# Kernel tuning notes

Hardware: AMD Instinct MI355X
Metric: run time of the kernel (lower is better)

The kernel has to match this reference:

```python
import jax, jax.numpy as jnp
import numpy as np

NUM_CLASSES = 80
TOPK = 13          # TaskAlignedAssigner topk
TAL_ALPHA = 1.0    # alignment = score^alpha * iou^beta
TAL_BETA = 6.0
VFL_ALPHA = 0.75   # varifocal loss
VFL_GAMMA = 2.0
CLS_W, IOU_W = 1.0, 2.5
EPS = 1e-9


def batch_iou(box1, box2, eps=1e-9):
    """box1 [B,M1,4], box2 [B,M2,4] (xyxy) -> iou [B,M1,M2]."""
    b1 = box1[:, :, None, :]
    b2 = box2[:, None, :, :]
    x1y1 = jnp.maximum(b1[..., :2], b2[..., :2])
    x2y2 = jnp.minimum(b1[..., 2:], b2[..., 2:])
    overlap = jnp.clip(x2y2 - x1y1, 0).prod(-1)
    area1 = jnp.clip(b1[..., 2:] - b1[..., :2], 0).prod(-1)
    area2 = jnp.clip(b2[..., 2:] - b2[..., :2], 0).prod(-1)
    return overlap / (area1 + area2 - overlap + eps)


def check_points_inside(points, bboxes, eps=EPS):
    """points [L,2], bboxes [B,n,4] -> [B,n,L] float (1 = anchor center inside gt)."""
    x = points[None, None, :, 0]
    y = points[None, None, :, 1]
    xmin, ymin, xmax, ymax = (bboxes[..., i:i + 1] for i in range(4))
    inside = jnp.minimum(jnp.minimum(x - xmin, y - ymin),
                         jnp.minimum(xmax - x, ymax - y)) > eps
    return inside.astype(bboxes.dtype)


def giou_loss(pb, gb, eps=1e-10):
    """Elementwise 1 - GIoU for xyxy boxes [..., 4]."""
    px1, py1, px2, py2 = (pb[..., i] for i in range(4))
    gx1, gy1, gx2, gy2 = (gb[..., i] for i in range(4))
    x1 = jnp.maximum(px1, gx1); y1 = jnp.maximum(py1, gy1)
    x2 = jnp.minimum(px2, gx2); y2 = jnp.minimum(py2, gy2)
    overlap = jnp.clip(x2 - x1, 0) * jnp.clip(y2 - y1, 0)
    area_p = jnp.clip(px2 - px1, 0) * jnp.clip(py2 - py1, 0)
    area_g = jnp.clip(gx2 - gx1, 0) * jnp.clip(gy2 - gy1, 0)
    union = area_p + area_g - overlap + eps
    iou = overlap / union
    cx1 = jnp.minimum(px1, gx1); cy1 = jnp.minimum(py1, gy1)
    cx2 = jnp.maximum(px2, gx2); cy2 = jnp.maximum(py2, gy2)
    c = jnp.clip(cx2 - cx1, 0) * jnp.clip(cy2 - cy1, 0) + eps
    return 1.0 - (iou - (c - union) / c)


def task_aligned_assign(pred_scores, pred_bboxes, anchor_points,
                        gt_labels, gt_bboxes, pad_gt_mask):
    """TaskAlignedAssigner.forward (no-grad in torch). Returns assigned
    labels [B,L], bboxes [B,L,4], scores [B,L,C], pos mask [B,L] float."""
    B, L, C = pred_scores.shape
    n = gt_bboxes.shape[1]
    ious = batch_iou(gt_bboxes, pred_bboxes)                       # [B,n,L]
    gl = gt_labels[..., 0]                                         # [B,n]
    # gather predicted class prob for each gt's class -> [B,n,L]
    scores_gt = jnp.take_along_axis(jnp.swapaxes(pred_scores, 1, 2),
                                    gl[:, :, None], axis=1)
    align = (scores_gt ** TAL_ALPHA) * (ious ** TAL_BETA)          # [B,n,L]
    is_in_gts = check_points_inside(anchor_points, gt_bboxes)      # [B,n,L]
    metrics = align * is_in_gts
    _, topk_idxs = jax.lax.top_k(metrics, TOPK)                    # [B,n,K]
    b_idx = jnp.arange(B)[:, None, None]
    n_idx = jnp.arange(n)[None, :, None]
    is_in_topk = jnp.zeros_like(metrics).at[b_idx, n_idx, topk_idxs].set(1.0)
    is_in_topk = is_in_topk * pad_gt_mask
    mask_pos = is_in_topk * is_in_gts * pad_gt_mask                # [B,n,L]
    mps = mask_pos.sum(1)                                          # [B,L]
    # anchors matched to >1 gt: keep only the max-iou gt
    is_max_iou = jnp.swapaxes(
        jax.nn.one_hot(ious.argmax(1), n, dtype=ious.dtype), 1, 2) # [B,n,L]
    mask_pos = jnp.where((mps > 1)[:, None, :], is_max_iou, mask_pos)
    mps = mask_pos.sum(1)                                          # [B,L]
    agi = mask_pos.argmax(1)                                       # [B,L]
    bi = jnp.arange(B)[:, None]
    assigned_labels = jnp.where(mps > 0, gl[bi, agi], NUM_CLASSES)
    assigned_bboxes = gt_bboxes[bi, agi]                           # [B,L,4]
    assigned_scores = jax.nn.one_hot(assigned_labels, C + 1,
                                     dtype=pred_scores.dtype)[..., :C]
    # rescale by alignment metric
    align = align * mask_pos
    max_metrics = align.max(-1, keepdims=True)                     # [B,n,1]
    max_ious = (ious * mask_pos).max(-1, keepdims=True)            # [B,n,1]
    align = align / (max_metrics + EPS) * max_ious
    assigned_scores = assigned_scores * align.max(1)[..., None]
    pos = (mps > 0).astype(pred_scores.dtype)
    return assigned_labels, assigned_bboxes, assigned_scores, pos


def setup_inputs() -> dict:
    key = jax.random.key(0)
    ks = jax.random.split(key, 6)
    B, N, C = 32, 100, NUM_CLASSES
    # anchor centers for strides 8/16/32 on a 640x640 image -> L = 8400
    pts = []
    for s in (8, 16, 32):
        g = 640 // s
        xs = (np.arange(g, dtype=np.float32) + 0.5) * s
        xv, yv = np.meshgrid(xs, xs)
        pts.append(np.stack([xv.ravel(), yv.ravel()], -1))
    anchor_points = jnp.asarray(np.concatenate(pts, 0))            # [8400,2]
    L = anchor_points.shape[0]

    def rand_boxes(k, lead):
        k1, k2 = jax.random.split(k)
        cxy = jax.random.uniform(k1, lead + (2,)) * 640.0
        wh = jax.random.uniform(k2, lead + (2,)) * 120.0 + 8.0
        return jnp.clip(jnp.concatenate([cxy - wh / 2, cxy + wh / 2], -1), 0.0, 640.0)

    pred_scores = jax.random.uniform(ks[0], (B, L, C), minval=1e-4, maxval=1.0 - 1e-4)
    pred_bboxes = rand_boxes(ks[1], (B, L))
    gt_bboxes = rand_boxes(ks[2], (B, N))
    gt_labels = jax.random.randint(ks[3], (B, N, 1), 0, C)
    num_gt = jax.random.randint(ks[4], (B, 1, 1), 20, N + 1)
    pad_gt_mask = (jnp.arange(N)[None, :, None] < num_gt).astype(jnp.float32)
    return {"pred_scores": pred_scores, "pred_bboxes": pred_bboxes,
            "anchor_points": anchor_points, "gt_labels": gt_labels,
            "gt_bboxes": gt_bboxes, "pad_gt_mask": pad_gt_mask}


def reference(pred_scores, pred_bboxes, anchor_points, gt_labels, gt_bboxes, pad_gt_mask):
    # --- assignment (torch runs it under no_grad) ---
    al, ab, asc, pos = jax.tree_util.tree_map(
        jax.lax.stop_gradient,
        task_aligned_assign(jax.lax.stop_gradient(pred_scores),
                            jax.lax.stop_gradient(pred_bboxes),
                            anchor_points, gt_labels, gt_bboxes, pad_gt_mask))
    asc_sum = jnp.maximum(asc.sum(), 1.0)
    # --- varifocal classification loss ---
    one_hot_label = jax.nn.one_hot(al, NUM_CLASSES + 1, dtype=pred_scores.dtype)[..., :NUM_CLASSES]
    w = VFL_ALPHA * (pred_scores ** VFL_GAMMA) * (1.0 - one_hot_label) + asc * one_hot_label
    p = jnp.clip(pred_scores, EPS, 1.0 - EPS)
    bce = -(asc * jnp.log(p) + (1.0 - asc) * jnp.log1p(-p))
    loss_cls = (bce * w).sum() / asc_sum
    # --- GIoU bbox loss on positive anchors, score-weighted ---
    bbox_weight = asc.sum(-1) * pos                                # [B,L]
    loss_iou = (giou_loss(pred_bboxes, ab) * bbox_weight).sum() / asc_sum
    return CLS_W * loss_cls + IOU_W * loss_iou
```

## Files before the change

### kernel.cpp

```cpp
#include <hip/hip_runtime.h>

#define NB 32
#define NGT 100
#define NL 8400
#define NC 80
#define KTOP 13
#define MAXC 640
#define NROWS (NB * NL)
#define TK_BLOCKS (NB * NGT / 4)
#define F_BLOCKS 2048
#define CR_BLOCKS (NROWS / 256)
#define SC_BLOCKS_X 33
#define TOTAL4 ((unsigned)NROWS * 20)
#define LN2F 0.6931471805599453f

__device__ __forceinline__ float clamp0(float x) { return fmaxf(x, 0.f); }

__device__ __forceinline__ unsigned long long mkkey(float v, unsigned lowk) {
  return ((unsigned long long)__float_as_uint(v) << 32) | (unsigned long long)lowk;
}

__device__ __forceinline__ float fbg(float s) {
  float pcl = fminf(fmaxf(s, 1e-9f), 1.f - 1e-9f);
  float lp1 = __log2f(1.f - pcl) * LN2F;
  return -lp1 * 0.75f * s * s;
}

__device__ __forceinline__ void anchor_xy(int l, float& x, float& y) {
  if (l < 6400)      { int rr = l / 80, cc = l - rr * 80;
                       x = ((float)cc + 0.5f) * 8.f;  y = ((float)rr + 0.5f) * 8.f; }
  else if (l < 8000) { int id = l - 6400; int rr = id / 40, cc = id - rr * 40;
                       x = ((float)cc + 0.5f) * 16.f; y = ((float)rr + 0.5f) * 16.f; }
  else               { int id = l - 8000; int rr = id / 20, cc = id - rr * 20;
                       x = ((float)cc + 0.5f) * 32.f; y = ((float)rr + 0.5f) * 32.f; }
}

__device__ __forceinline__ double block_red(double v, double* sred) {
  for (int off = 32; off > 0; off >>= 1) v += __shfl_down(v, off);
  int wid = threadIdx.x >> 6;
  if ((threadIdx.x & 63) == 0) sred[wid] = v;
  __syncthreads();
  double r = 0.0;
  if (threadIdx.x == 0) r = sred[0] + sred[1] + sred[2] + sred[3];
  __syncthreads();
  return r;
}

__device__ __forceinline__ void grange(float lo, float hi, float s, int G,
                                       int& a0, int& an) {
  int c0 = max(0, (int)floorf(lo / s - 0.5f));
  int c1 = min(G - 1, (int)ceilf(hi / s - 0.5f));
  a0 = c0;
  an = max(0, c1 - c0 + 1);
}

__global__ __launch_bounds__(256) void combo_kernel(
    const float* __restrict__ ps, const float* __restrict__ pb,
    const int* __restrict__ gl, const float* __restrict__ gtb,
    int* __restrict__ topk_out, unsigned* __restrict__ maxm,
    unsigned* __restrict__ maxi, double* __restrict__ partF)
{
  __shared__ unsigned long long cand[4][MAXC];
  __shared__ int cnt[4];
  __shared__ double sred[4];

  if (blockIdx.x >= TK_BLOCKS) {
    const int fb = blockIdx.x - TK_BLOCKS;
    const float4* ps4 = (const float4*)ps;
    double acc = 0.0;
    for (unsigned gid = (unsigned)fb * 256 + threadIdx.x; gid < TOTAL4;
         gid += (unsigned)F_BLOCKS * 256) {
      float4 s4 = ps4[gid];
      acc += (double)(fbg(s4.x) + fbg(s4.y) + fbg(s4.z) + fbg(s4.w));
    }
    double r = block_red(acc, sred);
    if (threadIdx.x == 0) partF[fb] = r;
    return;
  }

  const int wid = (int)(threadIdx.x >> 6);
  const int lane = (int)(threadIdx.x & 63);
  const int bn = blockIdx.x * 4 + wid;
  const int b = bn / NGT;
  const float gx1 = gtb[bn * 4 + 0], gy1 = gtb[bn * 4 + 1];
  const float gx2 = gtb[bn * 4 + 2], gy2 = gtb[bn * 4 + 3];
  const int cls = gl[bn];
  const float ga = clamp0(gx2 - gx1) * clamp0(gy2 - gy1);
  const float4* pbb = (const float4*)pb + (size_t)b * NL;
  const float* psb = ps + (size_t)b * NL * NC;

  if (lane == 0) {
    cnt[wid] = 0;
    maxm[bn] = 0u;
    maxi[bn] = 0u;
  }

  unsigned long long zm;
  {
    const int l = lane;
    float4 p = pbb[l];
    float x = ((float)l + 0.5f) * 8.0f, y = 4.0f;
    float ox = fminf(p.z, gx2) - fmaxf(p.x, gx1);
    float oy = fminf(p.w, gy2) - fmaxf(p.y, gy1);
    float ov = clamp0(ox) * clamp0(oy);
    float pa = clamp0(p.z - p.x) * clamp0(p.w - p.y);
    float iou = ov * __builtin_amdgcn_rcpf(ga + pa - ov + 1e-9f);
    bool ins = fminf(fminf(x - gx1, y - gy1),
                     fminf(gx2 - x, gy2 - y)) > 1e-9f;
    bool pos = ins && (iou > 0.f);
    zm = __ballot(!pos);
  }

  int c8, nc8, r8, nr8, c16, nc16, r16, nr16, c32, nc32, r32, nr32;
  grange(gx1, gx2, 8.f, 80, c8, nc8);   grange(gy1, gy2, 8.f, 80, r8, nr8);
  grange(gx1, gx2, 16.f, 40, c16, nc16); grange(gy1, gy2, 16.f, 40, r16, nr16);
  grange(gx1, gx2, 32.f, 20, c32, nc32); grange(gy1, gy2, 32.f, 20, r32, nr32);
  const int t8 = nc8 * nr8, t16 = nc16 * nr16, t32 = nc32 * nr32;
  const int total = t8 + t16 + t32;

  for (int idx = lane; idx < total; idx += 64) {
    int l; float x, y;
    if (idx < t8) {
      int q = idx / nc8, cc = c8 + (idx - q * nc8), rr = r8 + q;
      l = rr * 80 + cc; x = ((float)cc + 0.5f) * 8.f; y = ((float)rr + 0.5f) * 8.f;
    } else if (idx < t8 + t16) {
      int id = idx - t8;
      int q = id / nc16, cc = c16 + (id - q * nc16), rr = r16 + q;
      l = 6400 + rr * 40 + cc; x = ((float)cc + 0.5f) * 16.f; y = ((float)rr + 0.5f) * 16.f;
    } else {
      int id = idx - t8 - t16;
      int q = id / nc32, cc = c32 + (id - q * nc32), rr = r32 + q;
      l = 8000 + rr * 20 + cc; x = ((float)cc + 0.5f) * 32.f; y = ((float)rr + 0.5f) * 32.f;
    }
    float4 p = pbb[l];
    float ox = fminf(p.z, gx2) - fmaxf(p.x, gx1);
    float oy = fminf(p.w, gy2) - fmaxf(p.y, gy1);
    float ov = clamp0(ox) * clamp0(oy);
    float pa = clamp0(p.z - p.x) * clamp0(p.w - p.y);
    float iou = ov * __builtin_amdgcn_rcpf(ga + pa - ov + 1e-9f);
    bool ins = fminf(fminf(x - gx1, y - gy1),
                     fminf(gx2 - x, gy2 - y)) > 1e-9f;
    if (ins && iou > 0.f) {
      int id2 = atomicAdd(&cnt[wid], 1);
      if (id2 < MAXC)
        cand[wid][id2] = ((unsigned long long)__float_as_uint(iou) << 32) |
                         (unsigned long long)(0xFFFFFFFFu - (unsigned)l);
    }
  }

  const int n = min(cnt[wid], MAXC);
  unsigned long long zadd = 0ull;
  for (int idx = lane; idx < n; idx += 64) {
    unsigned long long e = cand[wid][idx];
    unsigned lowk = (unsigned)e;
    int l = (int)(0xFFFFFFFFu - lowk);
    float iou = __uint_as_float((unsigned)(e >> 32));
    float sc = psb[(size_t)l * NC + cls];
    float i2 = iou * iou;
    float v = sc * i2 * i2 * i2;
    if (v > 0.f) {
      cand[wid][idx] = mkkey(v, lowk);
    } else {
      cand[wid][idx] = 0ull;
      if (l < 64) zadd |= (1ull << l);
    }
  }
  for (int off = 1; off < 64; off <<= 1)
    zadd |= __shfl_xor(zadd, off);
  zm |= zadd;

  unsigned long long c[MAXC / 64];
#pragma unroll
  for (int j = 0; j < MAXC / 64; ++j) {
    int idx = lane + 64 * j;
    c[j] = (idx < n) ? cand[wid][idx] : 0ull;
  }
  for (int k = 0; k < KTOP; ++k) {
    unsigned long long m = c[0];
#pragma unroll
    for (int j = 1; j < MAXC / 64; ++j) m = (c[j] > m) ? c[j] : m;
    for (int off = 1; off < 64; off <<= 1) {
      unsigned long long o = __shfl_xor(m, off);
      m = (o > m) ? o : m;
    }
    int outl;
    if (m != 0ull) {
#pragma unroll
      for (int j = 0; j < MAXC / 64; ++j)
        if (c[j] == m) c[j] = 0ull;
      outl = (int)(0xFFFFFFFFu - (unsigned)(m & 0xFFFFFFFFull));
    } else {
      outl = (int)(__ffsll((long long)zm) - 1);
      zm &= zm - 1;
    }
    if (lane == 0) topk_out[bn * KTOP + k] = outl;
  }
}

__global__ __launch_bounds__(256) void assign_kernel(
    const float* __restrict__ ps, const float* __restrict__ pb,
    const int* __restrict__ gl, const float* __restrict__ gtb,
    const float* __restrict__ pad, const int* __restrict__ topk,
    int* __restrict__ nstar, float* __restrict__ astar,
    unsigned* __restrict__ maxm, unsigned* __restrict__ maxi)
{
  __shared__ float4 sgt[NGT];
  __shared__ int sgl[NGT];
  __shared__ float spad[NGT];
  __shared__ unsigned hitm[256][4];
  const int b = blockIdx.y;
  const int l0 = blockIdx.x * 256;

  for (int i = threadIdx.x; i < NGT; i += 256) {
    sgt[i] = ((const float4*)gtb)[b * NGT + i];
    sgl[i] = gl[b * NGT + i];
    spad[i] = pad[b * NGT + i];
  }
  hitm[threadIdx.x][0] = 0u; hitm[threadIdx.x][1] = 0u;
  hitm[threadIdx.x][2] = 0u; hitm[threadIdx.x][3] = 0u;
  __syncthreads();

  for (int i = threadIdx.x; i < NGT * KTOP; i += 256) {
    const int n = i / KTOP;
    if (spad[n] == 0.f) continue;
    const int l = topk[b * NGT * KTOP + i];
    if (l < l0 || l >= l0 + 256 || l >= NL) continue;
    float ax, ay;
    anchor_xy(l, ax, ay);
    float4 g = sgt[n];
    bool ins = fminf(fminf(ax - g.x, ay - g.y),
                     fminf(g.z - ax, g.w - ay)) > 1e-9f;
    if (ins) atomicOr(&hitm[l - l0][n >> 5], 1u << (n & 31));
  }
  __syncthreads();

  const int l = l0 + threadIdx.x;
  if (l >= NL) return;

  const unsigned m0 = hitm[threadIdx.x][0], m1 = hitm[threadIdx.x][1];
  const unsigned m2 = hitm[threadIdx.x][2], m3 = hitm[threadIdx.x][3];
  const int mps = __popc(m0) + __popc(m1) + __popc(m2) + __popc(m3);

  int ns = -1;
  float iou_s = 0.f, al_s = 0.f;
  if (mps > 0) {
    float4 p = ((const float4*)pb)[(size_t)b * NL + l];
    float pa = clamp0(p.z - p.x) * clamp0(p.w - p.y);
    if (mps == 1) {
      if (m0) ns = __ffs(m0) - 1;
      else if (m1) ns = 32 + __ffs(m1) - 1;
      else if (m2) ns = 64 + __ffs(m2) - 1;
      else ns = 96 + __ffs(m3) - 1;
      float4 g = sgt[ns];
      float ox = fminf(p.z, g.z) - fmaxf(p.x, g.x);
      float oy = fminf(p.w, g.w) - fmaxf(p.y, g.y);
      float ov = clamp0(ox) * clamp0(oy);
      float ga = clamp0(g.z - g.x) * clamp0(g.w - g.y);
      iou_s = ov / (ga + pa - ov + 1e-9f);
    } else {
      int max_n = 0; float max_iou = -1.f;
      for (int n = 0; n < NGT; ++n) {
        float4 g = sgt[n];
        float ox = fminf(p.z, g.z) - fmaxf(p.x, g.x);
        float oy = fminf(p.w, g.w) - fmaxf(p.y, g.y);
        float ov = clamp0(ox) * clamp0(oy);
        float ga = clamp0(g.z - g.x) * clamp0(g.w - g.y);
        float iou = ov / (ga + pa - ov + 1e-9f);
        if (iou > max_iou) { max_iou = iou; max_n = n; }
      }
      ns = max_n; iou_s = max_iou;
    }
    float sc = ps[((size_t)b * NL + l) * NC + sgl[ns]];
    float i2 = iou_s * iou_s;
    al_s = sc * i2 * i2 * i2;
    atomicMax(&maxm[b * NGT + ns], __float_as_uint(al_s));
    atomicMax(&maxi[b * NGT + ns], __float_as_uint(iou_s));
  }
  nstar[b * NL + l] = ns;
  astar[b * NL + l] = al_s;
}

__global__ __launch_bounds__(256) void correct_kernel(
    const float* __restrict__ ps, const float* __restrict__ pb,
    const float* __restrict__ gtb, const int* __restrict__ gl,
    const int* __restrict__ nstar, const float* __restrict__ astar,
    const unsigned* __restrict__ maxm, const unsigned* __restrict__ maxi,
    double* __restrict__ partC)
{
  __shared__ double sred[4];
  const int row = blockIdx.x * 256 + threadIdx.x;
  const int b = row / NL;
  double csum = 0.0, gsum = 0.0, asum = 0.0;
  int ns = nstar[row];
  if (ns >= 0) {
    float mm = __uint_as_float(maxm[b * NGT + ns]);
    float mi = __uint_as_float(maxi[b * NGT + ns]);
    float scale = astar[row] / (mm + 1e-9f) * mi;
    int j = gl[b * NGT + ns];
    asum = (double)scale;
    float s = ps[(size_t)row * NC + j];
    float pcl = fminf(fmaxf(s, 1e-9f), 1.f - 1e-9f);
    float lp1 = __log2f(1.f - pcl) * LN2F;
    float lpp = __log2f(pcl) * LN2F;
    float term = -(scale * lpp + (1.f - scale) * lp1) * scale;
    float fsj = -lp1 * 0.75f * s * s;
    csum = (double)(term - fsj);
    float4 p = ((const float4*)pb)[row];
    float4 g = ((const float4*)gtb)[b * NGT + ns];
    float x1 = fmaxf(p.x, g.x), y1 = fmaxf(p.y, g.y);
    float x2 = fminf(p.z, g.z), y2 = fminf(p.w, g.w);
    float ov = clamp0(x2 - x1) * clamp0(y2 - y1);
    float pa = clamp0(p.z - p.x) * clamp0(p.w - p.y);
    float ga = clamp0(g.z - g.x) * clamp0(g.w - g.y);
    float un = pa + ga - ov + 1e-10f;
    float iou = ov / un;
    float cx1 = fminf(p.x, g.x), cy1 = fminf(p.y, g.y);
    float cx2 = fmaxf(p.z, g.z), cy2 = fmaxf(p.w, g.w);
    float cc = clamp0(cx2 - cx1) * clamp0(cy2 - cy1) + 1e-10f;
    float gi = 1.f - (iou - (cc - un) / cc);
    gsum = (double)(gi * scale);
  }
  double r0 = block_red(csum, sred);
  double r1 = block_red(gsum, sred);
  double r2 = block_red(asum, sred);
  if (threadIdx.x == 0) {
    partC[(size_t)blockIdx.x * 4 + 0] = r0;
    partC[(size_t)blockIdx.x * 4 + 1] = r1;
    partC[(size_t)blockIdx.x * 4 + 2] = r2;
  }
}

__global__ __launch_bounds__(256) void fin_kernel(
    const double* __restrict__ partF, const double* __restrict__ partC,
    float* __restrict__ out)
{
  __shared__ double sred[4];
  double c = 0.0, g = 0.0, a = 0.0;
  for (int i = threadIdx.x; i < F_BLOCKS; i += 256) c += partF[i];
  for (int i = threadIdx.x; i < CR_BLOCKS; i += 256) {
    c += partC[(size_t)i * 4 + 0];
    g += partC[(size_t)i * 4 + 1];
    a += partC[(size_t)i * 4 + 2];
  }
  c = block_red(c, sred);
  g = block_red(g, sred);
  a = block_red(a, sred);
  if (threadIdx.x == 0) {
    double s = a > 1.0 ? a : 1.0;
    out[0] = (float)((c + 2.5 * g) / s);
  }
}

extern "C" void kernel_launch(void* const* d_in, const int* in_sizes, int n_in,
                              void* d_out, int out_size, void* d_ws, size_t ws_size,
                              hipStream_t stream) {
  const float* ps  = (const float*)d_in[0];
  const float* pbx = (const float*)d_in[1];
  const float* ap  = (const float*)d_in[2];
  const int*   gl  = (const int*)d_in[3];
  const float* gtb = (const float*)d_in[4];
  const float* pad = (const float*)d_in[5];
  (void)ap;

  char* ws = (char*)d_ws;
  const size_t OFF_MAXM  = 0;
  const size_t OFF_MAXI  = OFF_MAXM + 4ul * NB * NGT;
  const size_t OFF_TOPK  = OFF_MAXI + 4ul * NB * NGT;
  const size_t OFF_NSTAR = OFF_TOPK + 4ul * NB * NGT * KTOP;
  const size_t OFF_ASTAR = OFF_NSTAR + 4ul * NB * NL;
  const size_t OFF_PARTF = OFF_ASTAR + 4ul * NB * NL;
  const size_t OFF_PARTC = OFF_PARTF + 8ul * F_BLOCKS;

  unsigned* maxm  = (unsigned*)(ws + OFF_MAXM);
  unsigned* maxi  = (unsigned*)(ws + OFF_MAXI);
  int*      topk  = (int*)(ws + OFF_TOPK);
  int*      nstar = (int*)(ws + OFF_NSTAR);
  float*    astar = (float*)(ws + OFF_ASTAR);
  double*   partF = (double*)(ws + OFF_PARTF);
  double*   partC = (double*)(ws + OFF_PARTC);


  hipLaunchKernelGGL(combo_kernel, dim3(TK_BLOCKS + F_BLOCKS), dim3(256), 0,
                     stream, ps, pbx, gl, gtb, topk, maxm, maxi, partF);
  hipLaunchKernelGGL(assign_kernel, dim3(SC_BLOCKS_X, NB), dim3(256), 0, stream,
                     ps, pbx, gl, gtb, pad, topk, nstar, astar, maxm, maxi);
  hipLaunchKernelGGL(correct_kernel, dim3(CR_BLOCKS), dim3(256), 0, stream,
                     ps, pbx, gtb, gl, nstar, astar, maxm, maxi, partC);
  hipLaunchKernelGGL(fin_kernel, dim3(1), dim3(256), 0, stream, partF, partC,
                     (float*)d_out);
}
```

Before: 67.66 us.

## Fuse assign and correct kernels into one per-batch block using shared memory

Merges the assign and correct kernels into one kernel with a 1024-thread block per batch image. Per-anchor assignment (ns, alignment) and the per-GT max alignment and IoU now live in shared memory instead of global workspace arrays. This removes one launch, the global nstar/astar round trip, the global atomics and the maxm/maxi zeroing. In exchange only 32 blocks run on a many-CU GPU, so each block works serially over 9 chunks, which lowers parallelism for that stage.

```diff
diff --git a/kernel.cpp b/kernel.cpp
--- a/kernel.cpp
+++ b/kernel.cpp
@@ -9,9 +9,9 @@
 #define NROWS (NB * NL)
 #define TK_BLOCKS (NB * NGT / 4)
 #define F_BLOCKS 2048
-#define CR_BLOCKS (NROWS / 256)
-#define SC_BLOCKS_X 33
 #define TOTAL4 ((unsigned)NROWS * 20)
+#define BT 1024
+#define NCHUNK ((NL + BT - 1) / BT)
 #define LN2F 0.6931471805599453f
 
 __device__ __forceinline__ float clamp0(float x) { return fmaxf(x, 0.f); }
@@ -46,6 +46,18 @@
   return r;
 }
 
+__device__ __forceinline__ double block_red16(double v, double* sred) {
+  for (int off = 32; off > 0; off >>= 1) v += __shfl_down(v, off);
+  int wid = threadIdx.x >> 6;
+  if ((threadIdx.x & 63) == 0) sred[wid] = v;
+  __syncthreads();
+  double r = 0.0;
+  if (threadIdx.x == 0)
+    for (int i = 0; i < 16; ++i) r += sred[i];
+  __syncthreads();
+  return r;
+}
+
 __device__ __forceinline__ void grange(float lo, float hi, float s, int G,
                                        int& a0, int& an) {
   int c0 = max(0, (int)floorf(lo / s - 0.5f));
@@ -57,8 +69,7 @@
 __global__ __launch_bounds__(256) void combo_kernel(
     const float* __restrict__ ps, const float* __restrict__ pb,
     const int* __restrict__ gl, const float* __restrict__ gtb,
-    int* __restrict__ topk_out, unsigned* __restrict__ maxm,
-    unsigned* __restrict__ maxi, double* __restrict__ partF)
+    int* __restrict__ topk_out, double* __restrict__ partF)
 {
   __shared__ unsigned long long cand[4][MAXC];
   __shared__ int cnt[4];
@@ -89,11 +100,7 @@
   const float4* pbb = (const float4*)pb + (size_t)b * NL;
   const float* psb = ps + (size_t)b * NL * NC;
 
-  if (lane == 0) {
-    cnt[wid] = 0;
-    maxm[bn] = 0u;
-    maxi[bn] = 0u;
-  }
+  if (lane == 0) cnt[wid] = 0;
 
   unsigned long long zm;
   {
@@ -197,116 +204,117 @@
   }
 }
 
-__global__ __launch_bounds__(256) void assign_kernel(
+__global__ __launch_bounds__(BT) void batch_kernel(
     const float* __restrict__ ps, const float* __restrict__ pb,
     const int* __restrict__ gl, const float* __restrict__ gtb,
     const float* __restrict__ pad, const int* __restrict__ topk,
-    int* __restrict__ nstar, float* __restrict__ astar,
-    unsigned* __restrict__ maxm, unsigned* __restrict__ maxi)
+    double* __restrict__ partB)
 {
   __shared__ float4 sgt[NGT];
   __shared__ int sgl[NGT];
   __shared__ float spad[NGT];
-  __shared__ unsigned hitm[256][4];
-  const int b = blockIdx.y;
-  const int l0 = blockIdx.x * 256;
-
-  for (int i = threadIdx.x; i < NGT; i += 256) {
+  __shared__ unsigned smaxm[NGT], smaxi[NGT];
+  __shared__ short sns[NL];
+  __shared__ float sast[NL];
+  __shared__ unsigned hitm[BT][4];
+  __shared__ double sred[16];
+  const int b = blockIdx.x;
+  const float4* pbb = (const float4*)pb + (size_t)b * NL;
+  const float* psb = ps + (size_t)b * NL * NC;
+
+  for (int i = threadIdx.x; i < NGT; i += BT) {
     sgt[i] = ((const float4*)gtb)[b * NGT + i];
     sgl[i] = gl[b * NGT + i];
     spad[i] = pad[b * NGT + i];
-  }
-  hitm[threadIdx.x][0] = 0u; hitm[threadIdx.x][1] = 0u;
-  hitm[threadIdx.x][2] = 0u; hitm[threadIdx.x][3] = 0u;
-  __syncthreads();
-
-  for (int i = threadIdx.x; i < NGT * KTOP; i += 256) {
-    const int n = i / KTOP;
-    if (spad[n] == 0.f) continue;
-    const int l = topk[b * NGT * KTOP + i];
-    if (l < l0 || l >= l0 + 256 || l >= NL) continue;
-    float ax, ay;
-    anchor_xy(l, ax, ay);
-    float4 g = sgt[n];
-    bool ins = fminf(fminf(ax - g.x, ay - g.y),
-                     fminf(g.z - ax, g.w - ay)) > 1e-9f;
-    if (ins) atomicOr(&hitm[l - l0][n >> 5], 1u << (n & 31));
-  }
-  __syncthreads();
-
-  const int l = l0 + threadIdx.x;
-  if (l >= NL) return;
-
-  const unsigned m0 = hitm[threadIdx.x][0], m1 = hitm[threadIdx.x][1];
-  const unsigned m2 = hitm[threadIdx.x][2], m3 = hitm[threadIdx.x][3];
-  const int mps = __popc(m0) + __popc(m1) + __popc(m2) + __popc(m3);
-
-  int ns = -1;
-  float iou_s = 0.f, al_s = 0.f;
-  if (mps > 0) {
-    float4 p = ((const float4*)pb)[(size_t)b * NL + l];
-    float pa = clamp0(p.z - p.x) * clamp0(p.w - p.y);
-    if (mps == 1) {
-      if (m0) ns = __ffs(m0) - 1;
-      else if (m1) ns = 32 + __ffs(m1) - 1;
-      else if (m2) ns = 64 + __ffs(m2) - 1;
-      else ns = 96 + __ffs(m3) - 1;
-      float4 g = sgt[ns];
-      float ox = fminf(p.z, g.z) - fmaxf(p.x, g.x);
-      float oy = fminf(p.w, g.w) - fmaxf(p.y, g.y);
-      float ov = clamp0(ox) * clamp0(oy);
-      float ga = clamp0(g.z - g.x) * clamp0(g.w - g.y);
-      iou_s = ov / (ga + pa - ov + 1e-9f);
-    } else {
-      int max_n = 0; float max_iou = -1.f;
-      for (int n = 0; n < NGT; ++n) {
-        float4 g = sgt[n];
-        float ox = fminf(p.z, g.z) - fmaxf(p.x, g.x);
-        float oy = fminf(p.w, g.w) - fmaxf(p.y, g.y);
-        float ov = clamp0(ox) * clamp0(oy);
-        float ga = clamp0(g.z - g.x) * clamp0(g.w - g.y);
-        float iou = ov / (ga + pa - ov + 1e-9f);
-        if (iou > max_iou) { max_iou = iou; max_n = n; }
+    smaxm[i] = 0u;
+    smaxi[i] = 0u;
+  }
+  __syncthreads();
+
+  for (int ch = 0; ch < NCHUNK; ++ch) {
+    const int l0 = ch * BT;
+    hitm[threadIdx.x][0] = 0u; hitm[threadIdx.x][1] = 0u;
+    hitm[threadIdx.x][2] = 0u; hitm[threadIdx.x][3] = 0u;
+    __syncthreads();
+
+    for (int i = threadIdx.x; i < NGT * KTOP; i += BT) {
+      const int n = i / KTOP;
+      if (spad[n] == 0.f) continue;
+      const int l = topk[b * NGT * KTOP + i];
+      if (l < l0 || l >= l0 + BT || l >= NL) continue;
+      float ax, ay;
+      anchor_xy(l, ax, ay);
+      float4 g = sgt[n];
+      bool ins = fminf(fminf(ax - g.x, ay - g.y),
+                       fminf(g.z - ax, g.w - ay)) > 1e-9f;
+      if (ins) atomicOr(&hitm[l - l0][n >> 5], 1u << (n & 31));
+    }
+    __syncthreads();
+
+    const int l = l0 + (int)threadIdx.x;
+    if (l < NL) {
+      const unsigned m0 = hitm[threadIdx.x][0], m1 = hitm[threadIdx.x][1];
+      const unsigned m2 = hitm[threadIdx.x][2], m3 = hitm[threadIdx.x][3];
+      const int mps = __popc(m0) + __popc(m1) + __popc(m2) + __popc(m3);
+      int ns = -1;
+      float iou_s = 0.f, al_s = 0.f;
+      if (mps > 0) {
+        float4 p = pbb[l];
+        float pa = clamp0(p.z - p.x) * clamp0(p.w - p.y);
+        if (mps == 1) {
+          if (m0) ns = __ffs(m0) - 1;
+          else if (m1) ns = 32 + __ffs(m1) - 1;
+          else if (m2) ns = 64 + __ffs(m2) - 1;
+          else ns = 96 + __ffs(m3) - 1;
+          float4 g = sgt[ns];
+          float ox = fminf(p.z, g.z) - fmaxf(p.x, g.x);
+          float oy = fminf(p.w, g.w) - fmaxf(p.y, g.y);
+          float ov = clamp0(ox) * clamp0(oy);
+          float ga = clamp0(g.z - g.x) * clamp0(g.w - g.y);
+          iou_s = ov / (ga + pa - ov + 1e-9f);
+        } else {
+          int max_n = 0; float max_iou = -1.f;
+          for (int n = 0; n < NGT; ++n) {
+            float4 g = sgt[n];
+            float ox = fminf(p.z, g.z) - fmaxf(p.x, g.x);
+            float oy = fminf(p.w, g.w) - fmaxf(p.y, g.y);
+            float ov = clamp0(ox) * clamp0(oy);
+            float ga = clamp0(g.z - g.x) * clamp0(g.w - g.y);
+            float iou = ov / (ga + pa - ov + 1e-9f);
+            if (iou > max_iou) { max_iou = iou; max_n = n; }
+          }
+          ns = max_n; iou_s = max_iou;
+        }
+        float sc = psb[(size_t)l * NC + sgl[ns]];
+        float i2 = iou_s * iou_s;
+        al_s = sc * i2 * i2 * i2;
+        atomicMax(&smaxm[ns], __float_as_uint(al_s));
+        atomicMax(&smaxi[ns], __float_as_uint(iou_s));
       }
-      ns = max_n; iou_s = max_iou;
-    }
-    float sc = ps[((size_t)b * NL + l) * NC + sgl[ns]];
-    float i2 = iou_s * iou_s;
-    al_s = sc * i2 * i2 * i2;
-    atomicMax(&maxm[b * NGT + ns], __float_as_uint(al_s));
-    atomicMax(&maxi[b * NGT + ns], __float_as_uint(iou_s));
-  }
-  nstar[b * NL + l] = ns;
-  astar[b * NL + l] = al_s;
-}
-
-__global__ __launch_bounds__(256) void correct_kernel(
-    const float* __restrict__ ps, const float* __restrict__ pb,
-    const float* __restrict__ gtb, const int* __restrict__ gl,
-    const int* __restrict__ nstar, const float* __restrict__ astar,
-    const unsigned* __restrict__ maxm, const unsigned* __restrict__ maxi,
-    double* __restrict__ partC)
-{
-  __shared__ double sred[4];
-  const int row = blockIdx.x * 256 + threadIdx.x;
-  const int b = row / NL;
+      sns[l] = (short)ns;
+      sast[l] = al_s;
+    }
+    __syncthreads();
+  }
+
   double csum = 0.0, gsum = 0.0, asum = 0.0;
-  int ns = nstar[row];
-  if (ns >= 0) {
-    float mm = __uint_as_float(maxm[b * NGT + ns]);
-    float mi = __uint_as_float(maxi[b * NGT + ns]);
-    float scale = astar[row] / (mm + 1e-9f) * mi;
-    int j = gl[b * NGT + ns];
-    asum = (double)scale;
-    float s = ps[(size_t)row * NC + j];
+  for (int l = threadIdx.x; l < NL; l += BT) {
+    int ns = sns[l];
+    if (ns < 0) continue;
+    float mm = __uint_as_float(smaxm[ns]);
+    float mi = __uint_as_float(smaxi[ns]);
+    float scale = sast[l] / (mm + 1e-9f) * mi;
+    int j = sgl[ns];
+    asum += (double)scale;
+    float s = psb[(size_t)l * NC + j];
     float pcl = fminf(fmaxf(s, 1e-9f), 1.f - 1e-9f);
     float lp1 = __log2f(1.f - pcl) * LN2F;
     float lpp = __log2f(pcl) * LN2F;
     float term = -(scale * lpp + (1.f - scale) * lp1) * scale;
     float fsj = -lp1 * 0.75f * s * s;
-    csum = (double)(term - fsj);
-    float4 p = ((const float4*)pb)[row];
-    float4 g = ((const float4*)gtb)[b * NGT + ns];
+    csum += (double)(term - fsj);
+    float4 p = pbb[l];
+    float4 g = sgt[ns];
     float x1 = fmaxf(p.x, g.x), y1 = fmaxf(p.y, g.y);
     float x2 = fminf(p.z, g.z), y2 = fminf(p.w, g.w);
     float ov = clamp0(x2 - x1) * clamp0(y2 - y1);
@@ -318,29 +326,29 @@
     float cx2 = fmaxf(p.z, g.z), cy2 = fmaxf(p.w, g.w);
     float cc = clamp0(cx2 - cx1) * clamp0(cy2 - cy1) + 1e-10f;
     float gi = 1.f - (iou - (cc - un) / cc);
-    gsum = (double)(gi * scale);
-  }
-  double r0 = block_red(csum, sred);
-  double r1 = block_red(gsum, sred);
-  double r2 = block_red(asum, sred);
+    gsum += (double)(gi * scale);
+  }
+  double r0 = block_red16(csum, sred);
+  double r1 = block_red16(gsum, sred);
+  double r2 = block_red16(asum, sred);
   if (threadIdx.x == 0) {
-    partC[(size_t)blockIdx.x * 4 + 0] = r0;
-    partC[(size_t)blockIdx.x * 4 + 1] = r1;
-    partC[(size_t)blockIdx.x * 4 + 2] = r2;
+    partB[(size_t)b * 4 + 0] = r0;
+    partB[(size_t)b * 4 + 1] = r1;
+    partB[(size_t)b * 4 + 2] = r2;
   }
 }
 
 __global__ __launch_bounds__(256) void fin_kernel(
-    const double* __restrict__ partF, const double* __restrict__ partC,
+    const double* __restrict__ partF, const double* __restrict__ partB,
     float* __restrict__ out)
 {
   __shared__ double sred[4];
   double c = 0.0, g = 0.0, a = 0.0;
   for (int i = threadIdx.x; i < F_BLOCKS; i += 256) c += partF[i];
-  for (int i = threadIdx.x; i < CR_BLOCKS; i += 256) {
-    c += partC[(size_t)i * 4 + 0];
-    g += partC[(size_t)i * 4 + 1];
-    a += partC[(size_t)i * 4 + 2];
+  if (threadIdx.x < NB) {
+    c += partB[(size_t)threadIdx.x * 4 + 0];
+    g += partB[(size_t)threadIdx.x * 4 + 1];
+    a += partB[(size_t)threadIdx.x * 4 + 2];
   }
   c = block_red(c, sred);
   g = block_red(g, sred);
@@ -363,29 +371,18 @@
   (void)ap;
 
   char* ws = (char*)d_ws;
-  const size_t OFF_MAXM  = 0;
-  const size_t OFF_MAXI  = OFF_MAXM + 4ul * NB * NGT;
-  const size_t OFF_TOPK  = OFF_MAXI + 4ul * NB * NGT;
-  const size_t OFF_NSTAR = OFF_TOPK + 4ul * NB * NGT * KTOP;
-  const size_t OFF_ASTAR = OFF_NSTAR + 4ul * NB * NL;
-  const size_t OFF_PARTF = OFF_ASTAR + 4ul * NB * NL;
-  const size_t OFF_PARTC = OFF_PARTF + 8ul * F_BLOCKS;
-
-  unsigned* maxm  = (unsigned*)(ws + OFF_MAXM);
-  unsigned* maxi  = (unsigned*)(ws + OFF_MAXI);
+  const size_t OFF_TOPK  = 0;
+  const size_t OFF_PARTF = OFF_TOPK + 4ul * NB * NGT * KTOP;
+  const size_t OFF_PARTB = OFF_PARTF + 8ul * F_BLOCKS;
+
   int*      topk  = (int*)(ws + OFF_TOPK);
-  int*      nstar = (int*)(ws + OFF_NSTAR);
-  float*    astar = (float*)(ws + OFF_ASTAR);
   double*   partF = (double*)(ws + OFF_PARTF);
-  double*   partC = (double*)(ws + OFF_PARTC);
-
+  double*   partB = (double*)(ws + OFF_PARTB);
 
   hipLaunchKernelGGL(combo_kernel, dim3(TK_BLOCKS + F_BLOCKS), dim3(256), 0,
-                     stream, ps, pbx, gl, gtb, topk, maxm, maxi, partF);
-  hipLaunchKernelGGL(assign_kernel, dim3(SC_BLOCKS_X, NB), dim3(256), 0, stream,
-                     ps, pbx, gl, gtb, pad, topk, nstar, astar, maxm, maxi);
-  hipLaunchKernelGGL(correct_kernel, dim3(CR_BLOCKS), dim3(256), 0, stream,
-                     ps, pbx, gtb, gl, nstar, astar, maxm, maxi, partC);
-  hipLaunchKernelGGL(fin_kernel, dim3(1), dim3(256), 0, stream, partF, partC,
+                     stream, ps, pbx, gl, gtb, topk, partF);
+  hipLaunchKernelGGL(batch_kernel, dim3(NB), dim3(BT), 0, stream,
+                     ps, pbx, gl, gtb, pad, topk, partB);
+  hipLaunchKernelGGL(fin_kernel, dim3(1), dim3(256), 0, stream, partF, partB,
                      (float*)d_out);
 }
```

After: 264.3 us. 3.91x slower.
